# Kernel tuning notes

Hardware: AMD Instinct MI355X
Metric: run time of the kernel (lower is better)

Reference implementation:

```python
import jax, jax.numpy as jnp
import numpy as np

VDIM, HDIM, B = 128, 512, 512
EPS = 1e-5  # torch LayerNorm default


def _ln(x, g, b):
    m = x.mean(-1, keepdims=True)
    v = ((x - m) ** 2).mean(-1, keepdims=True)
    return (x - m) * jax.lax.rsqrt(v + EPS) * g + b


def setup_inputs() -> dict:
    key = jax.random.key(0)
    ks = jax.random.split(key, 16)
    s = 0.05  # small init so sigmoids/logs stay numerically tame
    d = {}
    d["u"] = jax.random.uniform(ks[0], (VDIM, B), jnp.float32)
    d["q_w1"] = s * jax.random.normal(ks[1], (VDIM, HDIM), jnp.float32)
    d["q_b1"] = jnp.zeros((HDIM,), jnp.float32)
    d["q_g1"] = jnp.ones((HDIM,), jnp.float32)
    d["q_be1"] = jnp.zeros((HDIM,), jnp.float32)
    d["q_w2"] = s * jax.random.normal(ks[2], (HDIM, HDIM), jnp.float32)
    d["q_b2"] = jnp.zeros((HDIM,), jnp.float32)
    d["q_g2"] = jnp.ones((HDIM,), jnp.float32)
    d["q_be2"] = jnp.zeros((HDIM,), jnp.float32)
    d["q_w3"] = s * jax.random.normal(ks[3], (HDIM, HDIM), jnp.float32)
    d["q_b3"] = jnp.zeros((HDIM,), jnp.float32)
    d["q_g3"] = jnp.ones((HDIM,), jnp.float32)
    d["q_be3"] = jnp.zeros((HDIM,), jnp.float32)
    d["q_W"] = 0.01 * jax.random.normal(ks[4], (VDIM, HDIM), jnp.float32)  # per-node output heads
    d["q_bias"] = jnp.zeros((VDIM,), jnp.float32)
    d["q_marg"] = jnp.zeros((VDIM,), jnp.float32)
    d["f_w1"] = s * jax.random.normal(ks[5], (VDIM, HDIM), jnp.float32)
    d["f_b1"] = jnp.zeros((HDIM,), jnp.float32)
    d["f_g1"] = jnp.ones((HDIM,), jnp.float32)
    d["f_be1"] = jnp.zeros((HDIM,), jnp.float32)
    d["f_w2"] = s * jax.random.normal(ks[6], (HDIM, HDIM), jnp.float32)
    d["f_b2"] = jnp.zeros((HDIM,), jnp.float32)
    d["f_g2"] = jnp.ones((HDIM,), jnp.float32)
    d["f_be2"] = jnp.zeros((HDIM,), jnp.float32)
    d["f_w3"] = s * jax.random.normal(ks[7], (HDIM, HDIM), jnp.float32)
    d["f_b3"] = jnp.zeros((HDIM,), jnp.float32)
    d["f_g3"] = jnp.ones((HDIM,), jnp.float32)
    d["f_be3"] = jnp.zeros((HDIM,), jnp.float32)
    d["f_w4"] = s * jax.random.normal(ks[8], (HDIM,), jnp.float32)
    d["f_b4"] = jnp.zeros((1,), jnp.float32)
    d["J"] = 0.1 * jax.random.normal(ks[9], (VDIM, VDIM), jnp.float32)  # Ising couplings for scorer
    d["top_order"] = jnp.arange(VDIM, dtype=jnp.int32)
    d["pa_mask"] = jax.random.randint(ks[10], (VDIM, VDIM), 0, 2, jnp.int32)
    return d


def reference(u, q_w1, q_b1, q_g1, q_be1, q_w2, q_b2, q_g2, q_be2,
              q_w3, q_b3, q_g3, q_be3, q_W, q_bias, q_marg,
              f_w1, f_b1, f_g1, f_be1, f_w2, f_b2, f_g2, f_be2,
              f_w3, f_b3, f_g3, f_be3, f_w4, f_b4, J,
              top_order, pa_mask):
    def qtrunk(V):
        h = jax.nn.relu(_ln(V @ q_w1 + q_b1, q_g1, q_be1))
        h = jax.nn.relu(_ln(h @ q_w2 + q_b2, q_g2, q_be2))
        h = jax.nn.relu(_ln(h @ q_w3 + q_b3, q_g3, q_be3))
        return h  # [B, H]

    def fnet(V):
        h = jax.nn.relu(_ln(V @ f_w1 + f_b1, f_g1, f_be1))
        h = jax.nn.relu(_ln(h @ f_w2 + f_b2, f_g2, f_be2))
        h = jax.nn.relu(_ln(h @ f_w3 + f_b3, f_g3, f_be3))
        return h @ f_w4 + f_b4[0]  # [B]

    # gather per-node quantities in topological order once, outside the scan
    masks = pa_mask[top_order].astype(u.dtype)          # [V, V] parent masks
    Wq = q_W[top_order]                                  # [V, H]
    bq = q_bias[top_order]                               # [V]
    mg = q_marg[top_order]                               # [V]
    oh = jax.nn.one_hot(top_order, VDIM, dtype=u.dtype)  # [V, V]

    def step(V, xs):
        mask_i, Wq_i, bq_i, mg_i, oh_i, u_i = xs
        V_pa = V * mask_i                                # [B, V] parents only
        x = qtrunk(V_pa) @ Wq_i + bq_i                   # [B]
        empty = jnp.abs(V_pa).sum(1) == 0
        p_on = jnp.where(empty, jax.nn.sigmoid(mg_i), jax.nn.sigmoid(x))
        samp = u_i < p_on                                # bernoulli(p_on)
        v_samp = 2.0 * samp.astype(u.dtype) - 1.0
        V_new = V * (1.0 - oh_i) + v_samp[:, None] * oh_i  # scatter into column
        lp = jnp.where(samp, jnp.log(p_on), jnp.log1p(-p_on))
        logF = fnet(jax.lax.stop_gradient(V_new))        # V.clone().detach()
        return V_new, (lp, logF)

    V0 = jnp.zeros((B, VDIM), u.dtype)
    V, (lps, logFs) = jax.lax.scan(step, V0, (masks, Wq, bq, mg, oh, u))
    log_pf = lps.T                                       # [B, V]
    F0 = fnet(V0)                                        # log_flow[:, 0] (alg='db')
    score = jax.lax.stop_gradient(jnp.einsum('bi,ij,bj->b', V, J, V))  # -energy, detached
    # last logF is overwritten by the terminal score, as in the original
    log_flow = jnp.concatenate([F0[:, None], logFs[:-1].T, score[:, None]], axis=1)  # [B, V+1]
    loss = ((log_flow[:, :-1] + log_pf - log_flow[:, 1:]) ** 2).mean(1).mean()
    return V, loss
```

## Files before the change

### kernel.cpp

```cpp
#include <hip/hip_runtime.h>
#include <hip/hip_bf16.h>
#include <math.h>

#define VDIM 128
#define HDIM 512
#define BATCH 512
#define RPB 4
#define NBLK (BATCH / RPB)
#define NT 512
#define LN_EPS 1e-5f

#define FNT 256
#define FROWS 16
#define FRG (BATCH / FROWS)
#define FGRID (VDIM * FRG)

__device__ __forceinline__ float4 f4zero() { return make_float4(0.f, 0.f, 0.f, 0.f); }
__device__ __forceinline__ float4 f4add(float4 a, float4 b) {
    return make_float4(a.x + b.x, a.y + b.y, a.z + b.z, a.w + b.w);
}
__device__ __forceinline__ float4 f4fma(float4 a, float s, float4 c) {
    return make_float4(fmaf(a.x, s, c.x), fmaf(a.y, s, c.y),
                       fmaf(a.z, s, c.z), fmaf(a.w, s, c.w));
}
__device__ __forceinline__ float4 f4scale(float4 a, float s) {
    return make_float4(a.x * s, a.y * s, a.z * s, a.w * s);
}
__device__ __forceinline__ float4 f4sub(float4 a, float4 b) {
    return make_float4(a.x - b.x, a.y - b.y, a.z - b.z, a.w - b.w);
}
__device__ __forceinline__ float f4get(float4 v, int r) {
    return r == 0 ? v.x : r == 1 ? v.y : r == 2 ? v.z : v.w;
}

struct Params {
    const float *u;
    const float *q_w1, *q_b1, *q_g1, *q_be1;
    const float *q_w2, *q_b2, *q_g2, *q_be2;
    const float *q_w3, *q_b3, *q_g3, *q_be3;
    const float *q_W, *q_bias, *q_marg;
    const float *f_w1, *f_b1, *f_g1, *f_be1;
    const float *f_w2, *f_b2, *f_g2, *f_be2;
    const float *f_w3, *f_b3, *f_g3, *f_be3;
    const float *f_w4, *f_b4, *J;
    const int *top_order, *pa_mask;
    float *V_out, *lp, *lf, *score, *vs, *loss;
};

__device__ __forceinline__ float4 allreduce4(float4 v, float4 *red4, int tid) {
#pragma unroll
    for (int off = 1; off < 64; off <<= 1) {
        v.x += __shfl_xor(v.x, off, 64);
        v.y += __shfl_xor(v.y, off, 64);
        v.z += __shfl_xor(v.z, off, 64);
        v.w += __shfl_xor(v.w, off, 64);
    }
    if ((tid & 63) == 0) red4[tid >> 6] = v;
    __syncthreads();
    float4 s = red4[0];
#pragma unroll
    for (int w = 1; w < 8; ++w) s = f4add(s, red4[w]);
    __syncthreads();
    return s;
}

__device__ __forceinline__ float block_reduce1(float v, float *red, int tid) {
#pragma unroll
    for (int off = 1; off < 64; off <<= 1) v += __shfl_xor(v, off, 64);
    if ((tid & 63) == 0) red[tid >> 6] = v;
    __syncthreads();
    float s = 0.f;
#pragma unroll
    for (int w = 0; w < 8; ++w) s += red[w];
    __syncthreads();
    return s;
}

template <int K>
__device__ __forceinline__ void gemv_ln_scan(const float4 *__restrict__ inAT,
                                             const float *__restrict__ W,
                                             const float *__restrict__ bias,
                                             const float *__restrict__ gam,
                                             const float *__restrict__ bet,
                                             float4 *__restrict__ outAT,
                                             float4 *part, float4 *red4,
                                             int tid, int ks, int cq) {
    const int kc = K / 4;
    const float4 *inP = inAT + ks * kc;
    const float4 *Wp = (const float4 *)W + (size_t)(ks * kc) * (HDIM / 4) + cq;
    float4 a0 = f4zero(), a1 = f4zero(), a2 = f4zero(), a3 = f4zero();
#pragma unroll 8
    for (int k = 0; k < kc; ++k) {
        float4 a = inP[k];
        float4 w = Wp[(size_t)k * (HDIM / 4)];
        a0 = f4fma(a, w.x, a0);
        a1 = f4fma(a, w.y, a1);
        a2 = f4fma(a, w.z, a2);
        a3 = f4fma(a, w.w, a3);
    }
    float4 *my = part + tid * 4;
    my[0] = a0; my[1] = a1; my[2] = a2; my[3] = a3;
    __syncthreads();
    float4 rowsum = f4zero();
    if (ks == 0) {
#pragma unroll
        for (int s = 1; s < 4; ++s) {
            const float4 *ps = part + (s * 128 + cq) * 4;
            a0 = f4add(a0, ps[0]);
            a1 = f4add(a1, ps[1]);
            a2 = f4add(a2, ps[2]);
            a3 = f4add(a3, ps[3]);
        }
        float4 b4 = ((const float4 *)bias)[cq];
        a0.x += b4.x; a0.y += b4.x; a0.z += b4.x; a0.w += b4.x;
        a1.x += b4.y; a1.y += b4.y; a1.z += b4.y; a1.w += b4.y;
        a2.x += b4.z; a2.y += b4.z; a2.z += b4.z; a2.w += b4.z;
        a3.x += b4.w; a3.y += b4.w; a3.z += b4.w; a3.w += b4.w;
        rowsum = f4add(f4add(a0, a1), f4add(a2, a3));
    }
    const float inv = 1.f / (float)HDIM;
    float4 m4 = f4scale(allreduce4(rowsum, red4, tid), inv);
    float4 d0, d1, d2, d3, sq = f4zero();
    if (ks == 0) {
        d0 = f4sub(a0, m4); d1 = f4sub(a1, m4);
        d2 = f4sub(a2, m4); d3 = f4sub(a3, m4);
        sq.x = d0.x * d0.x + d1.x * d1.x + d2.x * d2.x + d3.x * d3.x;
        sq.y = d0.y * d0.y + d1.y * d1.y + d2.y * d2.y + d3.y * d3.y;
        sq.z = d0.z * d0.z + d1.z * d1.z + d2.z * d2.z + d3.z * d3.z;
        sq.w = d0.w * d0.w + d1.w * d1.w + d2.w * d2.w + d3.w * d3.w;
    }
    float4 var = f4scale(allreduce4(sq, red4, tid), inv);
    if (ks == 0) {
        float4 rs;
        rs.x = 1.f / sqrtf(var.x + LN_EPS);
        rs.y = 1.f / sqrtf(var.y + LN_EPS);
        rs.z = 1.f / sqrtf(var.z + LN_EPS);
        rs.w = 1.f / sqrtf(var.w + LN_EPS);
        float4 g4 = ((const float4 *)gam)[cq];
        float4 e4 = ((const float4 *)bet)[cq];
        float4 h;
        h.x = fmaxf(fmaf(d0.x * rs.x, g4.x, e4.x), 0.f);
        h.y = fmaxf(fmaf(d0.y * rs.y, g4.x, e4.x), 0.f);
        h.z = fmaxf(fmaf(d0.z * rs.z, g4.x, e4.x), 0.f);
        h.w = fmaxf(fmaf(d0.w * rs.w, g4.x, e4.x), 0.f);
        outAT[4 * cq + 0] = h;
        h.x = fmaxf(fmaf(d1.x * rs.x, g4.y, e4.y), 0.f);
        h.y = fmaxf(fmaf(d1.y * rs.y, g4.y, e4.y), 0.f);
        h.z = fmaxf(fmaf(d1.z * rs.z, g4.y, e4.y), 0.f);
        h.w = fmaxf(fmaf(d1.w * rs.w, g4.y, e4.y), 0.f);
        outAT[4 * cq + 1] = h;
        h.x = fmaxf(fmaf(d2.x * rs.x, g4.z, e4.z), 0.f);
        h.y = fmaxf(fmaf(d2.y * rs.y, g4.z, e4.z), 0.f);
        h.z = fmaxf(fmaf(d2.z * rs.z, g4.z, e4.z), 0.f);
        h.w = fmaxf(fmaf(d2.w * rs.w, g4.z, e4.z), 0.f);
        outAT[4 * cq + 2] = h;
        h.x = fmaxf(fmaf(d3.x * rs.x, g4.w, e4.w), 0.f);
        h.y = fmaxf(fmaf(d3.y * rs.y, g4.w, e4.w), 0.f);
        h.z = fmaxf(fmaf(d3.z * rs.z, g4.w, e4.w), 0.f);
        h.w = fmaxf(fmaf(d3.w * rs.w, g4.w, e4.w), 0.f);
        outAT[4 * cq + 3] = h;
    }
    __syncthreads();
}

__global__ __launch_bounds__(NT) void gfn_scan(Params P) {
    __shared__ float4 VT[VDIM];
    __shared__ float4 VPT[VDIM];
    __shared__ float4 ATa[HDIM];
    __shared__ float4 ATb[HDIM];
    __shared__ float4 part[4 * 128 * 4];
    __shared__ float4 red4[8];

    const int tid = threadIdx.x;
    const int ks = tid >> 7;
    const int cq = tid & 127;
    const int row0 = blockIdx.x * RPB;

    if (tid < VDIM) VT[tid] = f4zero();
    __syncthreads();

    for (int i = 0; i < VDIM; ++i) {
        const int node = P.top_order[i];

        float4 ap = f4zero();
        if (tid < VDIM) {
            float mk = (float)P.pa_mask[node * VDIM + tid];
            float4 v = VT[tid];
            float4 vp = f4scale(v, mk);
            VPT[tid] = vp;
            ap = make_float4(fabsf(vp.x), fabsf(vp.y), fabsf(vp.z), fabsf(vp.w));
        }
        float4 asum = allreduce4(ap, red4, tid);

        gemv_ln_scan<VDIM>(VPT, P.q_w1, P.q_b1, P.q_g1, P.q_be1, ATa, part, red4, tid, ks, cq);
        gemv_ln_scan<HDIM>(ATa, P.q_w2, P.q_b2, P.q_g2, P.q_be2, ATb, part, red4, tid, ks, cq);
        gemv_ln_scan<HDIM>(ATb, P.q_w3, P.q_b3, P.q_g3, P.q_be3, ATa, part, red4, tid, ks, cq);

        float4 xp = f4zero();
        if (tid < 128) {
            float4 wq = ((const float4 *)(P.q_W + (size_t)node * HDIM))[tid];
            xp = f4fma(ATa[4 * tid + 0], wq.x, xp);
            xp = f4fma(ATa[4 * tid + 1], wq.y, xp);
            xp = f4fma(ATa[4 * tid + 2], wq.z, xp);
            xp = f4fma(ATa[4 * tid + 3], wq.w, xp);
        }
        float4 x4 = allreduce4(xp, red4, tid);

        if (tid < RPB) {
            const int r = tid;
            float asr = f4get(asum, r);
            float xr = f4get(x4, r) + P.q_bias[node];
            float arg = (asr == 0.f) ? P.q_marg[node] : xr;
            float p = 1.f / (1.f + expf(-arg));
            float uv = P.u[i * BATCH + row0 + r];
            bool samp = uv < p;
            float v = samp ? 1.f : -1.f;
            ((float *)&VT[node])[r] = v;
            P.vs[i * BATCH + row0 + r] = v;
            P.lp[i * BATCH + row0 + r] = samp ? logf(p) : log1pf(-p);
        }
        __syncthreads();
    }

    float4 inner = f4zero();
    if (tid < 128) {
#pragma unroll 4
        for (int ii = 0; ii < VDIM; ++ii)
            inner = f4fma(VT[ii], P.J[(size_t)ii * VDIM + tid], inner);
        float4 vc = VT[tid];
        inner = make_float4(inner.x * vc.x, inner.y * vc.y, inner.z * vc.z, inner.w * vc.w);
    }
    float4 sc4 = allreduce4(inner, red4, tid);
    if (tid < RPB) P.score[row0 + tid] = f4get(sc4, tid);
    if (tid < VDIM) {
        float4 v = VT[tid];
        P.V_out[(size_t)(row0 + 0) * VDIM + tid] = v.x;
        P.V_out[(size_t)(row0 + 1) * VDIM + tid] = v.y;
        P.V_out[(size_t)(row0 + 2) * VDIM + tid] = v.z;
        P.V_out[(size_t)(row0 + 3) * VDIM + tid] = v.w;
    }
}

__device__ __forceinline__ void reduce8_256(float4 &a, float4 &b,
                                            float4 *redA, float4 *redB, int tid) {
#pragma unroll
    for (int off = 1; off < 64; off <<= 1) {
        a.x += __shfl_xor(a.x, off, 64); a.y += __shfl_xor(a.y, off, 64);
        a.z += __shfl_xor(a.z, off, 64); a.w += __shfl_xor(a.w, off, 64);
        b.x += __shfl_xor(b.x, off, 64); b.y += __shfl_xor(b.y, off, 64);
        b.z += __shfl_xor(b.z, off, 64); b.w += __shfl_xor(b.w, off, 64);
    }
    int w = tid >> 6;
    if ((tid & 63) == 0) { redA[w] = a; redB[w] = b; }
    __syncthreads();
    int p = w ^ 1;
    a = f4add(redA[w], redA[p]);
    b = f4add(redB[w], redB[p]);
    __syncthreads();
}

template <int K>
__device__ __forceinline__ void flayer(const float *__restrict__ in,
                                       const float *__restrict__ W,
                                       const float *__restrict__ bias,
                                       const float *__restrict__ gam,
                                       const float *__restrict__ bet,
                                       float *__restrict__ out,
                                       float4 *redA, float4 *redB, int tid) {
    const int rh = tid >> 7, cq = tid & 127;
    const float4 *Wv = (const float4 *)W + cq;
    float4 accA[4], accB[4];
#pragma unroll
    for (int j = 0; j < 4; ++j) { accA[j] = f4zero(); accB[j] = f4zero(); }
#pragma unroll 4
    for (int k = 0; k < K; ++k) {
        float4 w = Wv[(size_t)k * (HDIM / 4)];
        const float *ip = in + k * FROWS + 8 * rh;
        float4 aA = *(const float4 *)ip;
        float4 aB = *(const float4 *)(ip + 4);
        accA[0] = f4fma(aA, w.x, accA[0]); accB[0] = f4fma(aB, w.x, accB[0]);
        accA[1] = f4fma(aA, w.y, accA[1]); accB[1] = f4fma(aB, w.y, accB[1]);
        accA[2] = f4fma(aA, w.z, accA[2]); accB[2] = f4fma(aB, w.z, accB[2]);
        accA[3] = f4fma(aA, w.w, accA[3]); accB[3] = f4fma(aB, w.w, accB[3]);
    }
    float4 b4 = ((const float4 *)bias)[cq];
    float bb[4] = {b4.x, b4.y, b4.z, b4.w};
#pragma unroll
    for (int j = 0; j < 4; ++j) {
        accA[j].x += bb[j]; accA[j].y += bb[j]; accA[j].z += bb[j]; accA[j].w += bb[j];
        accB[j].x += bb[j]; accB[j].y += bb[j]; accB[j].z += bb[j]; accB[j].w += bb[j];
    }
    const float inv = 1.f / (float)HDIM;
    float4 sA = f4add(f4add(accA[0], accA[1]), f4add(accA[2], accA[3]));
    float4 sB = f4add(f4add(accB[0], accB[1]), f4add(accB[2], accB[3]));
    reduce8_256(sA, sB, redA, redB, tid);
    float4 mA = f4scale(sA, inv), mB = f4scale(sB, inv);
    float4 dA[4], dB[4];
    float4 qA = f4zero(), qB = f4zero();
#pragma unroll
    for (int j = 0; j < 4; ++j) {
        dA[j] = f4sub(accA[j], mA);
        dB[j] = f4sub(accB[j], mB);
        qA.x += dA[j].x * dA[j].x; qA.y += dA[j].y * dA[j].y;
        qA.z += dA[j].z * dA[j].z; qA.w += dA[j].w * dA[j].w;
        qB.x += dB[j].x * dB[j].x; qB.y += dB[j].y * dB[j].y;
        qB.z += dB[j].z * dB[j].z; qB.w += dB[j].w * dB[j].w;
    }
    reduce8_256(qA, qB, redA, redB, tid);
    float4 rsA, rsB;
    rsA.x = 1.f / sqrtf(qA.x * inv + LN_EPS); rsA.y = 1.f / sqrtf(qA.y * inv + LN_EPS);
    rsA.z = 1.f / sqrtf(qA.z * inv + LN_EPS); rsA.w = 1.f / sqrtf(qA.w * inv + LN_EPS);
    rsB.x = 1.f / sqrtf(qB.x * inv + LN_EPS); rsB.y = 1.f / sqrtf(qB.y * inv + LN_EPS);
    rsB.z = 1.f / sqrtf(qB.z * inv + LN_EPS); rsB.w = 1.f / sqrtf(qB.w * inv + LN_EPS);
    float4 g4 = ((const float4 *)gam)[cq];
    float4 e4 = ((const float4 *)bet)[cq];
    float gg[4] = {g4.x, g4.y, g4.z, g4.w};
    float ee[4] = {e4.x, e4.y, e4.z, e4.w};
#pragma unroll
    for (int j = 0; j < 4; ++j) {
        float4 hA, hB;
        hA.x = fmaxf(fmaf(dA[j].x * rsA.x, gg[j], ee[j]), 0.f);
        hA.y = fmaxf(fmaf(dA[j].y * rsA.y, gg[j], ee[j]), 0.f);
        hA.z = fmaxf(fmaf(dA[j].z * rsA.z, gg[j], ee[j]), 0.f);
        hA.w = fmaxf(fmaf(dA[j].w * rsA.w, gg[j], ee[j]), 0.f);
        hB.x = fmaxf(fmaf(dB[j].x * rsB.x, gg[j], ee[j]), 0.f);
        hB.y = fmaxf(fmaf(dB[j].y * rsB.y, gg[j], ee[j]), 0.f);
        hB.z = fmaxf(fmaf(dB[j].z * rsB.z, gg[j], ee[j]), 0.f);
        hB.w = fmaxf(fmaf(dB[j].w * rsB.w, gg[j], ee[j]), 0.f);
        float *op = out + (4 * cq + j) * FROWS + 8 * rh;
        *(float4 *)op = hA;
        *(float4 *)(op + 4) = hB;
    }
    __syncthreads();
}

__global__ __launch_bounds__(FNT) void gfn_fnet(Params P) {
    __shared__ float Vt[VDIM * FROWS];
    __shared__ float A[HDIM * FROWS];
    __shared__ int ord[VDIM];
    __shared__ int invp[VDIM];
    __shared__ float4 redA[4], redB[4];

    const int tid = threadIdx.x;
    const int t = blockIdx.x >> 5;
    const int r0 = (blockIdx.x & 31) * FROWS;

    if (tid < VDIM) ord[tid] = P.top_order[tid];
    __syncthreads();
    if (tid < VDIM) invp[ord[tid]] = tid;
    __syncthreads();
    for (int idx = tid; idx < VDIM * FROWS; idx += FNT) {
        int k = idx >> 4, row = idx & 15;
        int s = invp[k];
        Vt[idx] = (s <= t) ? P.vs[s * BATCH + r0 + row] : 0.f;
    }
    __syncthreads();

    flayer<VDIM>(Vt, P.f_w1, P.f_b1, P.f_g1, P.f_be1, A, redA, redB, tid);
    flayer<HDIM>(A, P.f_w2, P.f_b2, P.f_g2, P.f_be2, A, redA, redB, tid);
    flayer<HDIM>(A, P.f_w3, P.f_b3, P.f_g3, P.f_be3, A, redA, redB, tid);

    const int rh = tid >> 7, cq = tid & 127;
    float4 w4 = ((const float4 *)P.f_w4)[cq];
    float ww[4] = {w4.x, w4.y, w4.z, w4.w};
    float4 sA = f4zero(), sB = f4zero();
#pragma unroll
    for (int j = 0; j < 4; ++j) {
        const float *ap = A + (4 * cq + j) * FROWS + 8 * rh;
        float4 aA = *(const float4 *)ap;
        float4 aB = *(const float4 *)(ap + 4);
        sA = f4fma(aA, ww[j], sA);
        sB = f4fma(aB, ww[j], sB);
    }
    reduce8_256(sA, sB, redA, redB, tid);
    if (cq == 0) {
        float b4v = P.f_b4[0];
        float *dst = P.lf + (size_t)t * BATCH + r0 + 8 * rh;
        dst[0] = sA.x + b4v; dst[1] = sA.y + b4v;
        dst[2] = sA.z + b4v; dst[3] = sA.w + b4v;
        dst[4] = sB.x + b4v; dst[5] = sB.y + b4v;
        dst[6] = sB.z + b4v; dst[7] = sB.w + b4v;
    }
}

__global__ __launch_bounds__(NT) void gfn_loss(Params P) {
    __shared__ float H1[HDIM], H2[HDIM];
    __shared__ float red1[8];
    const int tid = threadIdx.x;
    const float inv = 1.f / (float)HDIM;

    float z = P.f_b1[tid];
    float m = block_reduce1(z, red1, tid) * inv;
    float d = z - m;
    float var = block_reduce1(d * d, red1, tid) * inv;
    float h = fmaxf(fmaf(d * (1.f / sqrtf(var + LN_EPS)), P.f_g1[tid], P.f_be1[tid]), 0.f);
    H1[tid] = h;
    __syncthreads();

    float acc = 0.f;
    for (int k = 0; k < HDIM; ++k) acc = fmaf(H1[k], P.f_w2[(size_t)k * HDIM + tid], acc);
    z = acc + P.f_b2[tid];
    m = block_reduce1(z, red1, tid) * inv;
    d = z - m;
    var = block_reduce1(d * d, red1, tid) * inv;
    h = fmaxf(fmaf(d * (1.f / sqrtf(var + LN_EPS)), P.f_g2[tid], P.f_be2[tid]), 0.f);
    H2[tid] = h;
    __syncthreads();

    acc = 0.f;
    for (int k = 0; k < HDIM; ++k) acc = fmaf(H2[k], P.f_w3[(size_t)k * HDIM + tid], acc);
    z = acc + P.f_b3[tid];
    m = block_reduce1(z, red1, tid) * inv;
    d = z - m;
    var = block_reduce1(d * d, red1, tid) * inv;
    h = fmaxf(fmaf(d * (1.f / sqrtf(var + LN_EPS)), P.f_g3[tid], P.f_be3[tid]), 0.f);
    float F0 = block_reduce1(h * P.f_w4[tid], red1, tid) + P.f_b4[0];

    const int b = tid;
    float lfp = F0;
    float s = 0.f;
    for (int t = 0; t < VDIM; ++t) {
        float lp = P.lp[t * BATCH + b];
        float lfn = (t == VDIM - 1) ? P.score[b] : P.lf[t * BATCH + b];
        float dd = lfp + lp - lfn;
        s = fmaf(dd, dd, s);
        lfp = lfn;
    }
    s *= (1.f / (float)VDIM);
    float total = block_reduce1(s, red1, tid) * (1.f / (float)BATCH);
    if (tid == 0) P.loss[0] = total;
}

extern "C" void kernel_launch(void *const *d_in, const int *in_sizes, int n_in,
                              void *d_out, int out_size, void *d_ws, size_t ws_size,
                              hipStream_t stream) {
    Params P;
    P.u     = (const float *)d_in[0];
    P.q_w1  = (const float *)d_in[1];
    P.q_b1  = (const float *)d_in[2];
    P.q_g1  = (const float *)d_in[3];
    P.q_be1 = (const float *)d_in[4];
    P.q_w2  = (const float *)d_in[5];
    P.q_b2  = (const float *)d_in[6];
    P.q_g2  = (const float *)d_in[7];
    P.q_be2 = (const float *)d_in[8];
    P.q_w3  = (const float *)d_in[9];
    P.q_b3  = (const float *)d_in[10];
    P.q_g3  = (const float *)d_in[11];
    P.q_be3 = (const float *)d_in[12];
    P.q_W   = (const float *)d_in[13];
    P.q_bias= (const float *)d_in[14];
    P.q_marg= (const float *)d_in[15];
    P.f_w1  = (const float *)d_in[16];
    P.f_b1  = (const float *)d_in[17];
    P.f_g1  = (const float *)d_in[18];
    P.f_be1 = (const float *)d_in[19];
    P.f_w2  = (const float *)d_in[20];
    P.f_b2  = (const float *)d_in[21];
    P.f_g2  = (const float *)d_in[22];
    P.f_be2 = (const float *)d_in[23];
    P.f_w3  = (const float *)d_in[24];
    P.f_b3  = (const float *)d_in[25];
    P.f_g3  = (const float *)d_in[26];
    P.f_be3 = (const float *)d_in[27];
    P.f_w4  = (const float *)d_in[28];
    P.f_b4  = (const float *)d_in[29];
    P.J     = (const float *)d_in[30];
    P.top_order = (const int *)d_in[31];
    P.pa_mask   = (const int *)d_in[32];

    float *ws = (float *)d_ws;
    P.V_out = (float *)d_out;
    P.loss  = (float *)d_out + (size_t)BATCH * VDIM;
    P.lp    = ws;
    P.lf    = ws + (size_t)VDIM * BATCH;
    P.score = ws + 2 * (size_t)VDIM * BATCH;
    P.vs    = ws + 2 * (size_t)VDIM * BATCH + BATCH;

    gfn_scan<<<dim3(NBLK), dim3(NT), 0, stream>>>(P);
    gfn_fnet<<<dim3(FGRID), dim3(FNT), 0, stream>>>(P);
    gfn_loss<<<dim3(1), dim3(NT), 0, stream>>>(P);
}
```

Measured before the change: 4.538 ms.

## Repartition scan GEMV into 8 K-slices with prefetched weights and all-thread LayerNorm

The per-step GEMV in the sequential scan kernel now splits K across 8 slices of 64 threads. Each thread covers two column quads (64 apart) and keeps a small rotating prefetch buffer of weight loads to hide global latency. The partial-sum reduction and LayerNorm epilogue are spread across all 512 threads, one output column each, instead of only the first 128. This shortens the serial per-layer critical path, at the cost of more registers and an 8-way shared-memory partial reduction.

New measurement: 4.705 ms. 3.7% more time.

```diff
diff --git a/kernel.cpp b/kernel.cpp
--- a/kernel.cpp
+++ b/kernel.cpp
@@ -9,6 +9,7 @@
 #define NBLK (BATCH / RPB)
 #define NT 512
 #define LN_EPS 1e-5f
+#define PF 4
 
 #define FNT 256
 #define FROWS 16
@@ -83,83 +84,77 @@
                                              const float *__restrict__ gam,
                                              const float *__restrict__ bet,
                                              float4 *__restrict__ outAT,
-                                             float4 *part, float4 *red4,
+                                             float4 (*partA)[8][64],
+                                             float4 (*partB)[8][64],
+                                             float4 *red4,
                                              int tid, int ks, int cq) {
-    const int kc = K / 4;
+    const int kc = K / 8;
     const float4 *inP = inAT + ks * kc;
-    const float4 *Wp = (const float4 *)W + (size_t)(ks * kc) * (HDIM / 4) + cq;
-    float4 a0 = f4zero(), a1 = f4zero(), a2 = f4zero(), a3 = f4zero();
-#pragma unroll 8
-    for (int k = 0; k < kc; ++k) {
+    const float4 *Wk = (const float4 *)W + (size_t)(ks * kc) * (HDIM / 4) + cq;
+
+    float4 acA0 = f4zero(), acA1 = f4zero(), acA2 = f4zero(), acA3 = f4zero();
+    float4 acB0 = f4zero(), acB1 = f4zero(), acB2 = f4zero(), acB3 = f4zero();
+
+    float4 wA[PF], wB[PF];
+#pragma unroll
+    for (int p = 0; p < PF; ++p) {
+        wA[p] = Wk[(size_t)p * (HDIM / 4)];
+        wB[p] = Wk[(size_t)p * (HDIM / 4) + 64];
+    }
+#pragma unroll 4
+    for (int k = 0; k < kc - PF; ++k) {
+        const int p = k & (PF - 1);
         float4 a = inP[k];
-        float4 w = Wp[(size_t)k * (HDIM / 4)];
-        a0 = f4fma(a, w.x, a0);
-        a1 = f4fma(a, w.y, a1);
-        a2 = f4fma(a, w.z, a2);
-        a3 = f4fma(a, w.w, a3);
-    }
-    float4 *my = part + tid * 4;
-    my[0] = a0; my[1] = a1; my[2] = a2; my[3] = a3;
-    __syncthreads();
-    float4 rowsum = f4zero();
-    if (ks == 0) {
-#pragma unroll
-        for (int s = 1; s < 4; ++s) {
-            const float4 *ps = part + (s * 128 + cq) * 4;
-            a0 = f4add(a0, ps[0]);
-            a1 = f4add(a1, ps[1]);
-            a2 = f4add(a2, ps[2]);
-            a3 = f4add(a3, ps[3]);
-        }
-        float4 b4 = ((const float4 *)bias)[cq];
-        a0.x += b4.x; a0.y += b4.x; a0.z += b4.x; a0.w += b4.x;
-        a1.x += b4.y; a1.y += b4.y; a1.z += b4.y; a1.w += b4.y;
-        a2.x += b4.z; a2.y += b4.z; a2.z += b4.z; a2.w += b4.z;
-        a3.x += b4.w; a3.y += b4.w; a3.z += b4.w; a3.w += b4.w;
-        rowsum = f4add(f4add(a0, a1), f4add(a2, a3));
-    }
+        float4 cA = wA[p], cB = wB[p];
+        wA[p] = Wk[(size_t)(k + PF) * (HDIM / 4)];
+        wB[p] = Wk[(size_t)(k + PF) * (HDIM / 4) + 64];
+        acA0 = f4fma(a, cA.x, acA0); acA1 = f4fma(a, cA.y, acA1);
+        acA2 = f4fma(a, cA.z, acA2); acA3 = f4fma(a, cA.w, acA3);
+        acB0 = f4fma(a, cB.x, acB0); acB1 = f4fma(a, cB.y, acB1);
+        acB2 = f4fma(a, cB.z, acB2); acB3 = f4fma(a, cB.w, acB3);
+    }
+#pragma unroll
+    for (int k = kc - PF; k < kc; ++k) {
+        const int p = k & (PF - 1);
+        float4 a = inP[k];
+        float4 cA = wA[p], cB = wB[p];
+        acA0 = f4fma(a, cA.x, acA0); acA1 = f4fma(a, cA.y, acA1);
+        acA2 = f4fma(a, cA.z, acA2); acA3 = f4fma(a, cA.w, acA3);
+        acB0 = f4fma(a, cB.x, acB0); acB1 = f4fma(a, cB.y, acB1);
+        acB2 = f4fma(a, cB.z, acB2); acB3 = f4fma(a, cB.w, acB3);
+    }
+    partA[0][ks][cq] = acA0; partA[1][ks][cq] = acA1;
+    partA[2][ks][cq] = acA2; partA[3][ks][cq] = acA3;
+    partB[0][ks][cq] = acB0; partB[1][ks][cq] = acB1;
+    partB[2][ks][cq] = acB2; partB[3][ks][cq] = acB3;
+    __syncthreads();
+
+    const int jj = tid & 3;
+    const int cc4 = (tid >> 2) & 63;
+    float4 (*part)[8][64] = (tid < 256) ? partA : partB;
+    float4 acc = part[jj][0][cc4];
+#pragma unroll
+    for (int s = 1; s < 8; ++s) acc = f4add(acc, part[jj][s][cc4]);
+    float bc = bias[tid];
+    acc.x += bc; acc.y += bc; acc.z += bc; acc.w += bc;
+
     const float inv = 1.f / (float)HDIM;
-    float4 m4 = f4scale(allreduce4(rowsum, red4, tid), inv);
-    float4 d0, d1, d2, d3, sq = f4zero();
-    if (ks == 0) {
-        d0 = f4sub(a0, m4); d1 = f4sub(a1, m4);
-        d2 = f4sub(a2, m4); d3 = f4sub(a3, m4);
-        sq.x = d0.x * d0.x + d1.x * d1.x + d2.x * d2.x + d3.x * d3.x;
-        sq.y = d0.y * d0.y + d1.y * d1.y + d2.y * d2.y + d3.y * d3.y;
-        sq.z = d0.z * d0.z + d1.z * d1.z + d2.z * d2.z + d3.z * d3.z;
-        sq.w = d0.w * d0.w + d1.w * d1.w + d2.w * d2.w + d3.w * d3.w;
-    }
+    float4 m4 = f4scale(allreduce4(acc, red4, tid), inv);
+    float4 d = f4sub(acc, m4);
+    float4 sq = make_float4(d.x * d.x, d.y * d.y, d.z * d.z, d.w * d.w);
     float4 var = f4scale(allreduce4(sq, red4, tid), inv);
-    if (ks == 0) {
-        float4 rs;
-        rs.x = 1.f / sqrtf(var.x + LN_EPS);
-        rs.y = 1.f / sqrtf(var.y + LN_EPS);
-        rs.z = 1.f / sqrtf(var.z + LN_EPS);
-        rs.w = 1.f / sqrtf(var.w + LN_EPS);
-        float4 g4 = ((const float4 *)gam)[cq];
-        float4 e4 = ((const float4 *)bet)[cq];
-        float4 h;
-        h.x = fmaxf(fmaf(d0.x * rs.x, g4.x, e4.x), 0.f);
-        h.y = fmaxf(fmaf(d0.y * rs.y, g4.x, e4.x), 0.f);
-        h.z = fmaxf(fmaf(d0.z * rs.z, g4.x, e4.x), 0.f);
-        h.w = fmaxf(fmaf(d0.w * rs.w, g4.x, e4.x), 0.f);
-        outAT[4 * cq + 0] = h;
-        h.x = fmaxf(fmaf(d1.x * rs.x, g4.y, e4.y), 0.f);
-        h.y = fmaxf(fmaf(d1.y * rs.y, g4.y, e4.y), 0.f);
-        h.z = fmaxf(fmaf(d1.z * rs.z, g4.y, e4.y), 0.f);
-        h.w = fmaxf(fmaf(d1.w * rs.w, g4.y, e4.y), 0.f);
-        outAT[4 * cq + 1] = h;
-        h.x = fmaxf(fmaf(d2.x * rs.x, g4.z, e4.z), 0.f);
-        h.y = fmaxf(fmaf(d2.y * rs.y, g4.z, e4.z), 0.f);
-        h.z = fmaxf(fmaf(d2.z * rs.z, g4.z, e4.z), 0.f);
-        h.w = fmaxf(fmaf(d2.w * rs.w, g4.z, e4.z), 0.f);
-        outAT[4 * cq + 2] = h;
-        h.x = fmaxf(fmaf(d3.x * rs.x, g4.w, e4.w), 0.f);
-        h.y = fmaxf(fmaf(d3.y * rs.y, g4.w, e4.w), 0.f);
-        h.z = fmaxf(fmaf(d3.z * rs.z, g4.w, e4.w), 0.f);
-        h.w = fmaxf(fmaf(d3.w * rs.w, g4.w, e4.w), 0.f);
-        outAT[4 * cq + 3] = h;
-    }
+    float4 rs;
+    rs.x = 1.f / sqrtf(var.x + LN_EPS);
+    rs.y = 1.f / sqrtf(var.y + LN_EPS);
+    rs.z = 1.f / sqrtf(var.z + LN_EPS);
+    rs.w = 1.f / sqrtf(var.w + LN_EPS);
+    float gc = gam[tid], ec = bet[tid];
+    float4 h;
+    h.x = fmaxf(fmaf(d.x * rs.x, gc, ec), 0.f);
+    h.y = fmaxf(fmaf(d.y * rs.y, gc, ec), 0.f);
+    h.z = fmaxf(fmaf(d.z * rs.z, gc, ec), 0.f);
+    h.w = fmaxf(fmaf(d.w * rs.w, gc, ec), 0.f);
+    outAT[tid] = h;
     __syncthreads();
 }
 
@@ -168,12 +163,13 @@
     __shared__ float4 VPT[VDIM];
     __shared__ float4 ATa[HDIM];
     __shared__ float4 ATb[HDIM];
-    __shared__ float4 part[4 * 128 * 4];
+    __shared__ float4 partA[4][8][64];
+    __shared__ float4 partB[4][8][64];
     __shared__ float4 red4[8];
 
     const int tid = threadIdx.x;
-    const int ks = tid >> 7;
-    const int cq = tid & 127;
+    const int ks = tid >> 6;
+    const int cq = tid & 63;
     const int row0 = blockIdx.x * RPB;
 
     if (tid < VDIM) VT[tid] = f4zero();
@@ -192,18 +188,12 @@
         }
         float4 asum = allreduce4(ap, red4, tid);
 
-        gemv_ln_scan<VDIM>(VPT, P.q_w1, P.q_b1, P.q_g1, P.q_be1, ATa, part, red4, tid, ks, cq);
-        gemv_ln_scan<HDIM>(ATa, P.q_w2, P.q_b2, P.q_g2, P.q_be2, ATb, part, red4, tid, ks, cq);
-        gemv_ln_scan<HDIM>(ATb, P.q_w3, P.q_b3, P.q_g3, P.q_be3, ATa, part, red4, tid, ks, cq);
-
-        float4 xp = f4zero();
-        if (tid < 128) {
-            float4 wq = ((const float4 *)(P.q_W + (size_t)node * HDIM))[tid];
-            xp = f4fma(ATa[4 * tid + 0], wq.x, xp);
-            xp = f4fma(ATa[4 * tid + 1], wq.y, xp);
-            xp = f4fma(ATa[4 * tid + 2], wq.z, xp);
-            xp = f4fma(ATa[4 * tid + 3], wq.w, xp);
-        }
+        gemv_ln_scan<VDIM>(VPT, P.q_w1, P.q_b1, P.q_g1, P.q_be1, ATa, partA, partB, red4, tid, ks, cq);
+        gemv_ln_scan<HDIM>(ATa, P.q_w2, P.q_b2, P.q_g2, P.q_be2, ATb, partA, partB, red4, tid, ks, cq);
+        gemv_ln_scan<HDIM>(ATb, P.q_w3, P.q_b3, P.q_g3, P.q_be3, ATa, partA, partB, red4, tid, ks, cq);
+
+        float wq = P.q_W[(size_t)node * HDIM + tid];
+        float4 xp = f4scale(ATa[tid], wq);
         float4 x4 = allreduce4(xp, red4, tid);
 
         if (tid < RPB) {
```
